# Performance work log

Measured on AMD Instinct MI355X. Metric: run time of the kernel, lower is better.

The kernel has to match this reference:

```python
import jax, jax.numpy as jnp
import numpy as np


def setup_inputs() -> dict:
    key = jax.random.key(0)
    ks = jax.random.split(key, 12)
    N, F, H, E = 100000, 128, 128, 625000
    x = jax.random.normal(ks[0], (N, F), dtype=jnp.float32)
    edge_index = jax.random.randint(ks[1], (2, E), 0, N, dtype=jnp.int64)
    s1 = 1.0 / np.sqrt(2 * F)
    s2 = 1.0 / np.sqrt(H)
    W1 = jax.random.uniform(ks[2], (2 * F, H), jnp.float32, -s1, s1)
    b1 = jax.random.uniform(ks[3], (H,), jnp.float32, -s1, s1)
    W2 = jax.random.uniform(ks[4], (H, H), jnp.float32, -s2, s2)
    b2 = jax.random.uniform(ks[5], (H,), jnp.float32, -s2, s2)
    W3 = jax.random.uniform(ks[6], (H, H), jnp.float32, -s2, s2)
    b3 = jax.random.uniform(ks[7], (H,), jnp.float32, -s2, s2)
    W4 = jax.random.uniform(ks[8], (H, 1), jnp.float32, -s2, s2)
    b4 = jax.random.uniform(ks[9], (1,), jnp.float32, -s2, s2)
    return {"x": x, "edge_index": edge_index, "W1": W1, "b1": b1,
            "W2": W2, "b2": b2, "W3": W3, "b3": b3, "W4": W4, "b4": b4}


def reference(x, edge_index, W1, b1, W2, b2, W3, b3, W4, b4):
    # Gather endpoint features and concat -> [E, 2F]
    x_i = x[edge_index[0], :]
    x_j = x[edge_index[1], :]
    ef = jnp.concatenate([x_i, x_j], axis=-1)
    h = jax.nn.relu(ef @ W1 + b1)
    h = jax.nn.relu(h @ W2 + b2)
    h = jax.nn.relu(h @ W3 + b3)
    return jax.nn.sigmoid(h @ W4 + b4)  # [E, 1]
```

## Files before the change

### kernel.cpp

```cpp
#include <hip/hip_runtime.h>
#include <math.h>

typedef _Float16 half8 __attribute__((ext_vector_type(8)));
typedef _Float16 half4 __attribute__((ext_vector_type(4)));
typedef float f32x4 __attribute__((ext_vector_type(4)));

#define HDIM 128
#define WHALFS 65536
#define SCR_HALFS 2048
#define LDS_HALFS (WHALFS + 8 * SCR_HALFS)
#define LDS_BYTES (LDS_HALFS * 2)

__global__ __launch_bounds__(256) void prep_kernel(
    const float* __restrict__ x,  const float* __restrict__ W1,
    const float* __restrict__ W2, const float* __restrict__ W3,
    _Float16* __restrict__ xh,  _Float16* __restrict__ W1p,
    _Float16* __restrict__ W2p, _Float16* __restrict__ W3p, int NF)
{
    int bid = blockIdx.x;
    if (bid < 32) {
        int t = bid * 256 + threadIdx.x;
        const float* W; _Float16* Wp; int KS; int u;
        if (t < 4096)      { W = W1; Wp = W1p; KS = 8; u = t; }
        else if (t < 6144) { W = W2; Wp = W2p; KS = 4; u = t - 4096; }
        else               { W = W3; Wp = W3p; KS = 4; u = t - 6144; }
        int lane = u & 63;
        int fk   = u >> 6;
        int ks   = fk % KS;
        int ct   = fk / KS;
        int m    = ct * 16 + (lane & 15);
        int k0   = ks * 32 + (lane >> 4) * 8;
        half8 v;
        #pragma unroll
        for (int j = 0; j < 8; ++j) v[j] = (_Float16)W[(k0 + j) * HDIM + m];
        *(half8*)(Wp + (size_t)u * 8) = v;
    } else {
        long i = (long)(bid - 32) * 2048 + (long)threadIdx.x * 8;
        if (i + 8 <= (long)NF) {
            const float4* xf = (const float4*)(x + i);
            float4 f0 = xf[0], f1 = xf[1];
            half8 v;
            v[0] = (_Float16)f0.x; v[1] = (_Float16)f0.y;
            v[2] = (_Float16)f0.z; v[3] = (_Float16)f0.w;
            v[4] = (_Float16)f1.x; v[5] = (_Float16)f1.y;
            v[6] = (_Float16)f1.z; v[7] = (_Float16)f1.w;
            *(half8*)(xh + i) = v;
        }
    }
}

__device__ __forceinline__ void acc_bias_init(
    f32x4 (&acc)[2][8], const float* __restrict__ bias, int quad)
{
    #pragma unroll
    for (int ct = 0; ct < 8; ++ct) {
        float4 bv = *(const float4*)(bias + ct * 16 + quad * 4);
        f32x4 b = {bv.x, bv.y, bv.z, bv.w};
        acc[0][ct] = b;
        acc[1][ct] = b;
    }
}

__device__ __forceinline__ void epi_extract(
    f32x4 (&acc)[2][8], _Float16* __restrict__ scr, int l15, int quad, int sw,
    half8 (&bh)[2][4], const float* __restrict__ next_bias)
{
    #pragma unroll
    for (int nt = 0; nt < 2; ++nt) {
        #pragma unroll
        for (int ct = 0; ct < 8; ++ct) {
            half4 h;
            h[0] = (_Float16)fmaxf(acc[nt][ct][0], 0.f);
            h[1] = (_Float16)fmaxf(acc[nt][ct][1], 0.f);
            h[2] = (_Float16)fmaxf(acc[nt][ct][2], 0.f);
            h[3] = (_Float16)fmaxf(acc[nt][ct][3], 0.f);
            *(half4*)(scr + ((l15 * 128 + ct * 16 + quad * 4) ^ sw)) = h;
        }
        #pragma unroll
        for (int ks = 0; ks < 4; ++ks)
            bh[nt][ks] = *(const half8*)(scr + ((l15 * 128 + ks * 32 + quad * 8) ^ sw));
    }
    acc_bias_init(acc, next_bias, quad);
}

__device__ __forceinline__ void layer_mfma(
    f32x4 (&acc)[2][8], const _Float16* __restrict__ Wl,
    half8 (&bh)[2][4], int lane)
{
    #pragma unroll
    for (int ks = 0; ks < 4; ++ks) {
        #pragma unroll
        for (int ch = 0; ch < 2; ++ch) {
            half8 aw[4];
            #pragma unroll
            for (int c = 0; c < 4; ++c)
                aw[c] = *(const half8*)(Wl + ((size_t)(((ch * 4 + c) * 4 + ks) * 64 + lane)) * 8);
            #pragma unroll
            for (int nt = 0; nt < 2; ++nt)
                #pragma unroll
                for (int c = 0; c < 4; ++c)
                    acc[nt][ch * 4 + c] = __builtin_amdgcn_mfma_f32_16x16x32_f16(
                        aw[c], bh[nt][ks], acc[nt][ch * 4 + c], 0, 0, 0);
        }
    }
}

__global__ __launch_bounds__(512, 2) void edge_mlp_kernel(
    const int* __restrict__ ei, const _Float16* __restrict__ xh,
    const _Float16* __restrict__ wpack,
    const float* __restrict__ b1, const float* __restrict__ b2,
    const float* __restrict__ b3, const float* __restrict__ W4,
    const float* __restrict__ b4, float* __restrict__ out, int E)
{
    extern __shared__ _Float16 lds[];

    {
        float4* dst = (float4*)lds;
        const float4* src = (const float4*)wpack;
        #pragma unroll
        for (int i = 0; i < 16; ++i)
            dst[i * 512 + threadIdx.x] = src[i * 512 + threadIdx.x];
    }
    __syncthreads();

    const int tid  = threadIdx.x;
    const int wave = tid >> 6;
    const int lane = tid & 63;
    const int l15  = lane & 15;
    const int quad = lane >> 4;
    const int sw   = (l15 & 7) << 3;

    const _Float16* W1l = lds;
    const _Float16* W2l = lds + 32768;
    const _Float16* W3l = lds + 49152;
    _Float16* scr = lds + WHALFS + wave * SCR_HALFS;

    const int ntiles = (E + 255) >> 8;
    const float b4v = b4[0];

    for (int t = blockIdx.x; t < ntiles; t += gridDim.x) {
        const int base = t * 256 + wave * 32;

        int gi[2], gj[2];
        #pragma unroll
        for (int nt = 0; nt < 2; ++nt) {
            const int row = min(base + nt * 16 + l15, E - 1);
            gi[nt] = ei[row];
            gj[nt] = ei[E + row];
        }

        f32x4 acc[2][8];
        acc_bias_init(acc, b1, quad);

        half8 bef[2][4];

        #pragma unroll
        for (int nt = 0; nt < 2; ++nt) {
            const _Float16* pi = xh + (size_t)gi[nt] * HDIM;
            #pragma unroll
            for (int ks = 0; ks < 4; ++ks)
                bef[nt][ks] = *(const half8*)(pi + ks * 32 + quad * 8);
        }
        #pragma unroll
        for (int ks = 0; ks < 4; ++ks) {
            #pragma unroll
            for (int ch = 0; ch < 2; ++ch) {
                half8 aw[4];
                #pragma unroll
                for (int c = 0; c < 4; ++c)
                    aw[c] = *(const half8*)(W1l + ((size_t)(((ch * 4 + c) * 8 + ks) * 64 + lane)) * 8);
                #pragma unroll
                for (int nt = 0; nt < 2; ++nt)
                    #pragma unroll
                    for (int c = 0; c < 4; ++c)
                        acc[nt][ch * 4 + c] = __builtin_amdgcn_mfma_f32_16x16x32_f16(
                            aw[c], bef[nt][ks], acc[nt][ch * 4 + c], 0, 0, 0);
            }
        }

        #pragma unroll
        for (int nt = 0; nt < 2; ++nt) {
            const _Float16* pj = xh + (size_t)gj[nt] * HDIM;
            #pragma unroll
            for (int ks = 0; ks < 4; ++ks)
                bef[nt][ks] = *(const half8*)(pj + ks * 32 + quad * 8);
        }
        #pragma unroll
        for (int ks = 0; ks < 4; ++ks) {
            #pragma unroll
            for (int ch = 0; ch < 2; ++ch) {
                half8 aw[4];
                #pragma unroll
                for (int c = 0; c < 4; ++c)
                    aw[c] = *(const half8*)(W1l + ((size_t)(((ch * 4 + c) * 8 + 4 + ks) * 64 + lane)) * 8);
                #pragma unroll
                for (int nt = 0; nt < 2; ++nt)
                    #pragma unroll
                    for (int c = 0; c < 4; ++c)
                        acc[nt][ch * 4 + c] = __builtin_amdgcn_mfma_f32_16x16x32_f16(
                            aw[c], bef[nt][ks], acc[nt][ch * 4 + c], 0, 0, 0);
            }
        }

        half8 bh[2][4];
        epi_extract(acc, scr, l15, quad, sw, bh, b2);
        layer_mfma(acc, W2l, bh, lane);
        epi_extract(acc, scr, l15, quad, sw, bh, b3);
        layer_mfma(acc, W3l, bh, lane);

        #pragma unroll
        for (int nt = 0; nt < 2; ++nt) {
            float s = 0.f;
            #pragma unroll
            for (int ct = 0; ct < 8; ++ct) {
                float4 w4v = *(const float4*)(W4 + ct * 16 + quad * 4);
                s += fmaxf(acc[nt][ct][0], 0.f) * w4v.x;
                s += fmaxf(acc[nt][ct][1], 0.f) * w4v.y;
                s += fmaxf(acc[nt][ct][2], 0.f) * w4v.z;
                s += fmaxf(acc[nt][ct][3], 0.f) * w4v.w;
            }
            s += __shfl_xor(s, 16, 64);
            s += __shfl_xor(s, 32, 64);
            const int row = base + nt * 16 + l15;
            if (quad == 0 && row < E)
                out[row] = 1.f / (1.f + __expf(-(s + b4v)));
        }
    }
}

extern "C" void kernel_launch(void* const* d_in, const int* in_sizes, int n_in,
                              void* d_out, int out_size, void* d_ws, size_t ws_size,
                              hipStream_t stream)
{
    const float* x  = (const float*)d_in[0];
    const int*   ei = (const int*)d_in[1];
    const float* W1 = (const float*)d_in[2];
    const float* b1 = (const float*)d_in[3];
    const float* W2 = (const float*)d_in[4];
    const float* b2 = (const float*)d_in[5];
    const float* W3 = (const float*)d_in[6];
    const float* b3 = (const float*)d_in[7];
    const float* W4 = (const float*)d_in[8];
    const float* b4 = (const float*)d_in[9];
    float* out = (float*)d_out;

    const int NF = in_sizes[0];
    const int E  = out_size;

    _Float16* xh  = (_Float16*)d_ws;
    _Float16* W1p = xh + NF;
    _Float16* W2p = W1p + 32768;
    _Float16* W3p = W2p + 16384;

    const int xblocks = (NF + 2047) / 2048;
    prep_kernel<<<32 + xblocks, 256, 0, stream>>>(x, W1, W2, W3, xh, W1p, W2p, W3p, NF);

    hipFuncSetAttribute((const void*)edge_mlp_kernel,
                        hipFuncAttributeMaxDynamicSharedMemorySize, LDS_BYTES);
    edge_mlp_kernel<<<256, 512, LDS_BYTES, stream>>>(ei, xh, W1p,
                                                     b1, b2, b3, W4, b4, out, E);
}
```

Measured before the change: 192.1 us.

## Prefetch next tile's edge indices and source features during current tile MLP

Software-pipelines the persistent edge loop. The next tile's edge indices are loaded during layer 2, and its source-node feature rows during layer 3, so the gather latency overlaps MFMA work. MFMA blocks are wrapped in s_setprio to favour the matrix waves, and the x-to-fp16 conversion now uses 4 elements per thread with more blocks. Holding the prefetched features in registers raises register pressure, which at 512 threads and 2 blocks per unit could cause spills.

```diff
diff --git a/kernel.cpp b/kernel.cpp
--- a/kernel.cpp
+++ b/kernel.cpp
@@ -35,16 +35,13 @@
         for (int j = 0; j < 8; ++j) v[j] = (_Float16)W[(k0 + j) * HDIM + m];
         *(half8*)(Wp + (size_t)u * 8) = v;
     } else {
-        long i = (long)(bid - 32) * 2048 + (long)threadIdx.x * 8;
-        if (i + 8 <= (long)NF) {
-            const float4* xf = (const float4*)(x + i);
-            float4 f0 = xf[0], f1 = xf[1];
-            half8 v;
-            v[0] = (_Float16)f0.x; v[1] = (_Float16)f0.y;
-            v[2] = (_Float16)f0.z; v[3] = (_Float16)f0.w;
-            v[4] = (_Float16)f1.x; v[5] = (_Float16)f1.y;
-            v[6] = (_Float16)f1.z; v[7] = (_Float16)f1.w;
-            *(half8*)(xh + i) = v;
+        long i = ((long)(bid - 32) * 256 + threadIdx.x) * 4;
+        if (i + 4 <= (long)NF) {
+            float4 f = *(const float4*)(x + i);
+            half4 v;
+            v[0] = (_Float16)f.x; v[1] = (_Float16)f.y;
+            v[2] = (_Float16)f.z; v[3] = (_Float16)f.w;
+            *(half4*)(xh + i) = v;
         }
     }
 }
@@ -87,6 +84,7 @@
     f32x4 (&acc)[2][8], const _Float16* __restrict__ Wl,
     half8 (&bh)[2][4], int lane)
 {
+    __builtin_amdgcn_s_setprio(1);
     #pragma unroll
     for (int ks = 0; ks < 4; ++ks) {
         #pragma unroll
@@ -103,6 +101,31 @@
                         aw[c], bh[nt][ks], acc[nt][ch * 4 + c], 0, 0, 0);
         }
     }
+    __builtin_amdgcn_s_setprio(0);
+}
+
+__device__ __forceinline__ void layer1_half(
+    f32x4 (&acc)[2][8], const _Float16* __restrict__ W1l,
+    half8 (&bef)[2][4], int ks0, int lane)
+{
+    __builtin_amdgcn_s_setprio(1);
+    #pragma unroll
+    for (int ks = 0; ks < 4; ++ks) {
+        #pragma unroll
+        for (int ch = 0; ch < 2; ++ch) {
+            half8 aw[4];
+            #pragma unroll
+            for (int c = 0; c < 4; ++c)
+                aw[c] = *(const half8*)(W1l + ((size_t)(((ch * 4 + c) * 8 + ks0 + ks) * 64 + lane)) * 8);
+            #pragma unroll
+            for (int nt = 0; nt < 2; ++nt)
+                #pragma unroll
+                for (int c = 0; c < 4; ++c)
+                    acc[nt][ch * 4 + c] = __builtin_amdgcn_mfma_f32_16x16x32_f16(
+                        aw[c], bef[nt][ks], acc[nt][ch * 4 + c], 0, 0, 0);
+        }
+    }
+    __builtin_amdgcn_s_setprio(0);
 }
 
 __global__ __launch_bounds__(512, 2) void edge_mlp_kernel(
@@ -138,74 +161,68 @@
     const int ntiles = (E + 255) >> 8;
     const float b4v = b4[0];
 
+    int gi[2], gj[2];
+    half8 befi[2][4];
+    {
+        const int base0 = blockIdx.x * 256 + wave * 32;
+        #pragma unroll
+        for (int nt = 0; nt < 2; ++nt) {
+            const int row = min(base0 + nt * 16 + l15, E - 1);
+            gi[nt] = ei[row];
+            gj[nt] = ei[E + row];
+        }
+        #pragma unroll
+        for (int nt = 0; nt < 2; ++nt) {
+            const _Float16* pi = xh + (size_t)gi[nt] * HDIM;
+            #pragma unroll
+            for (int ks = 0; ks < 4; ++ks)
+                befi[nt][ks] = *(const half8*)(pi + ks * 32 + quad * 8);
+        }
+    }
+
     for (int t = blockIdx.x; t < ntiles; t += gridDim.x) {
         const int base = t * 256 + wave * 32;
 
-        int gi[2], gj[2];
-        #pragma unroll
-        for (int nt = 0; nt < 2; ++nt) {
-            const int row = min(base + nt * 16 + l15, E - 1);
-            gi[nt] = ei[row];
-            gj[nt] = ei[E + row];
+        half8 befj[2][4];
+        #pragma unroll
+        for (int nt = 0; nt < 2; ++nt) {
+            const _Float16* pj = xh + (size_t)gj[nt] * HDIM;
+            #pragma unroll
+            for (int ks = 0; ks < 4; ++ks)
+                befj[nt][ks] = *(const half8*)(pj + ks * 32 + quad * 8);
         }
 
         f32x4 acc[2][8];
         acc_bias_init(acc, b1, quad);
 
-        half8 bef[2][4];
-
-        #pragma unroll
-        for (int nt = 0; nt < 2; ++nt) {
-            const _Float16* pi = xh + (size_t)gi[nt] * HDIM;
-            #pragma unroll
-            for (int ks = 0; ks < 4; ++ks)
-                bef[nt][ks] = *(const half8*)(pi + ks * 32 + quad * 8);
-        }
-        #pragma unroll
-        for (int ks = 0; ks < 4; ++ks) {
-            #pragma unroll
-            for (int ch = 0; ch < 2; ++ch) {
-                half8 aw[4];
-                #pragma unroll
-                for (int c = 0; c < 4; ++c)
-                    aw[c] = *(const half8*)(W1l + ((size_t)(((ch * 4 + c) * 8 + ks) * 64 + lane)) * 8);
-                #pragma unroll
-                for (int nt = 0; nt < 2; ++nt)
-                    #pragma unroll
-                    for (int c = 0; c < 4; ++c)
-                        acc[nt][ch * 4 + c] = __builtin_amdgcn_mfma_f32_16x16x32_f16(
-                            aw[c], bef[nt][ks], acc[nt][ch * 4 + c], 0, 0, 0);
-            }
-        }
-
-        #pragma unroll
-        for (int nt = 0; nt < 2; ++nt) {
-            const _Float16* pj = xh + (size_t)gj[nt] * HDIM;
-            #pragma unroll
-            for (int ks = 0; ks < 4; ++ks)
-                bef[nt][ks] = *(const half8*)(pj + ks * 32 + quad * 8);
-        }
-        #pragma unroll
-        for (int ks = 0; ks < 4; ++ks) {
-            #pragma unroll
-            for (int ch = 0; ch < 2; ++ch) {
-                half8 aw[4];
-                #pragma unroll
-                for (int c = 0; c < 4; ++c)
-                    aw[c] = *(const half8*)(W1l + ((size_t)(((ch * 4 + c) * 8 + 4 + ks) * 64 + lane)) * 8);
-                #pragma unroll
-                for (int nt = 0; nt < 2; ++nt)
-                    #pragma unroll
-                    for (int c = 0; c < 4; ++c)
-                        acc[nt][ch * 4 + c] = __builtin_amdgcn_mfma_f32_16x16x32_f16(
-                            aw[c], bef[nt][ks], acc[nt][ch * 4 + c], 0, 0, 0);
-            }
-        }
+        layer1_half(acc, W1l, befi, 0, lane);
+        layer1_half(acc, W1l, befj, 4, lane);
 
         half8 bh[2][4];
         epi_extract(acc, scr, l15, quad, sw, bh, b2);
+
+        int gin[2], gjn[2];
+        {
+            const int basen = (t + (int)gridDim.x) * 256 + wave * 32;
+            #pragma unroll
+            for (int nt = 0; nt < 2; ++nt) {
+                const int row = min(min(basen + nt * 16 + l15, E - 1), E - 1);
+                gin[nt] = ei[row];
+                gjn[nt] = ei[E + row];
+            }
+        }
+
         layer_mfma(acc, W2l, bh, lane);
         epi_extract(acc, scr, l15, quad, sw, bh, b3);
+
+        #pragma unroll
+        for (int nt = 0; nt < 2; ++nt) {
+            const _Float16* pi = xh + (size_t)gin[nt] * HDIM;
+            #pragma unroll
+            for (int ks = 0; ks < 4; ++ks)
+                befi[nt][ks] = *(const half8*)(pi + ks * 32 + quad * 8);
+        }
+
         layer_mfma(acc, W3l, bh, lane);
 
         #pragma unroll
@@ -225,6 +242,9 @@
             if (quad == 0 && row < E)
                 out[row] = 1.f / (1.f + __expf(-(s + b4v)));
         }
+
+        gi[0] = gin[0]; gi[1] = gin[1];
+        gj[0] = gjn[0]; gj[1] = gjn[1];
     }
 }
 
@@ -252,7 +272,7 @@
     _Float16* W2p = W1p + 32768;
     _Float16* W3p = W2p + 16384;
 
-    const int xblocks = (NF + 2047) / 2048;
+    const int xblocks = (NF + 1023) / 1024;
     prep_kernel<<<32 + xblocks, 256, 0, stream>>>(x, W1, W2, W3, xh, W1p, W2p, W3p, NF);
 
     hipFuncSetAttribute((const void*)edge_mlp_kernel,
```

After: 201.0 us. 4.7% more time.

## Split output columns across wave pairs sharing 64-edge tiles in edge MLP

Applied to the files above, without the earlier changes.

Each pair of waves now processes 64 edges, with each wave computing half of the 128 output columns across four 16-row tiles. This halves the per-wave weight fragment loads from LDS per MFMA and raises B-operand reuse. The price is block-wide __syncthreads for the activation exchange and the final dot-product reduction, plus s_setprio hints around the MFMA loops. The prep kernel also becomes grid-stride with a fixed block count, and NF is hardcoded to the test shape.

```diff
diff --git a/kernel.cpp b/kernel.cpp
--- a/kernel.cpp
+++ b/kernel.cpp
@@ -7,8 +7,8 @@
 
 #define HDIM 128
 #define WHALFS 65536
-#define SCR_HALFS 2048
-#define LDS_HALFS (WHALFS + 8 * SCR_HALFS)
+#define PAIR_SCR_HALFS 4096
+#define LDS_HALFS (WHALFS + 4 * PAIR_SCR_HALFS)
 #define LDS_BYTES (LDS_HALFS * 2)
 
 __global__ __launch_bounds__(256) void prep_kernel(
@@ -35,8 +35,9 @@
         for (int j = 0; j < 8; ++j) v[j] = (_Float16)W[(k0 + j) * HDIM + m];
         *(half8*)(Wp + (size_t)u * 8) = v;
     } else {
-        long i = (long)(bid - 32) * 2048 + (long)threadIdx.x * 8;
-        if (i + 8 <= (long)NF) {
+        const long stride = (long)(gridDim.x - 32) * 256;
+        for (long u = (long)(bid - 32) * 256 + threadIdx.x; u * 8 < (long)NF; u += stride) {
+            long i = u * 8;
             const float4* xf = (const float4*)(x + i);
             float4 f0 = xf[0], f1 = xf[1];
             half8 v;
@@ -50,59 +51,91 @@
 }
 
 __device__ __forceinline__ void acc_bias_init(
-    f32x4 (&acc)[2][8], const float* __restrict__ bias, int quad)
-{
-    #pragma unroll
-    for (int ct = 0; ct < 8; ++ct) {
-        float4 bv = *(const float4*)(bias + ct * 16 + quad * 4);
+    f32x4 (&acc)[4][4], const float* __restrict__ bias, int h, int quad)
+{
+    #pragma unroll
+    for (int ct = 0; ct < 4; ++ct) {
+        float4 bv = *(const float4*)(bias + h * 64 + ct * 16 + quad * 4);
         f32x4 b = {bv.x, bv.y, bv.z, bv.w};
-        acc[0][ct] = b;
-        acc[1][ct] = b;
-    }
-}
-
-__device__ __forceinline__ void epi_extract(
-    f32x4 (&acc)[2][8], _Float16* __restrict__ scr, int l15, int quad, int sw,
-    half8 (&bh)[2][4], const float* __restrict__ next_bias)
-{
-    #pragma unroll
-    for (int nt = 0; nt < 2; ++nt) {
-        #pragma unroll
-        for (int ct = 0; ct < 8; ++ct) {
-            half4 h;
-            h[0] = (_Float16)fmaxf(acc[nt][ct][0], 0.f);
-            h[1] = (_Float16)fmaxf(acc[nt][ct][1], 0.f);
-            h[2] = (_Float16)fmaxf(acc[nt][ct][2], 0.f);
-            h[3] = (_Float16)fmaxf(acc[nt][ct][3], 0.f);
-            *(half4*)(scr + ((l15 * 128 + ct * 16 + quad * 4) ^ sw)) = h;
-        }
-        #pragma unroll
-        for (int ks = 0; ks < 4; ++ks)
-            bh[nt][ks] = *(const half8*)(scr + ((l15 * 128 + ks * 32 + quad * 8) ^ sw));
-    }
-    acc_bias_init(acc, next_bias, quad);
-}
-
-__device__ __forceinline__ void layer_mfma(
-    f32x4 (&acc)[2][8], const _Float16* __restrict__ Wl,
-    half8 (&bh)[2][4], int lane)
-{
+        #pragma unroll
+        for (int nt = 0; nt < 4; ++nt) acc[nt][ct] = b;
+    }
+}
+
+__device__ __forceinline__ void epi_extract_pair(
+    f32x4 (&acc)[4][4], _Float16* __restrict__ scr, int l15, int quad,
+    int h, int sw, half8 (&bh)[4][4], const float* __restrict__ next_bias)
+{
+    #pragma unroll
+    for (int g = 0; g < 2; ++g) {
+        #pragma unroll
+        for (int nl = 0; nl < 2; ++nl) {
+            const int nt = 2 * g + nl;
+            const int r  = nl * 16 + l15;
+            #pragma unroll
+            for (int ct = 0; ct < 4; ++ct) {
+                half4 hv;
+                hv[0] = (_Float16)fmaxf(acc[nt][ct][0], 0.f);
+                hv[1] = (_Float16)fmaxf(acc[nt][ct][1], 0.f);
+                hv[2] = (_Float16)fmaxf(acc[nt][ct][2], 0.f);
+                hv[3] = (_Float16)fmaxf(acc[nt][ct][3], 0.f);
+                *(half4*)(scr + ((r * 128 + h * 64 + ct * 16 + quad * 4) ^ sw)) = hv;
+            }
+        }
+        __syncthreads();
+        #pragma unroll
+        for (int nl = 0; nl < 2; ++nl) {
+            const int nt = 2 * g + nl;
+            const int r  = nl * 16 + l15;
+            #pragma unroll
+            for (int ks = 0; ks < 4; ++ks)
+                bh[nt][ks] = *(const half8*)(scr + ((r * 128 + ks * 32 + quad * 8) ^ sw));
+        }
+        __syncthreads();
+    }
+    acc_bias_init(acc, next_bias, h, quad);
+}
+
+__device__ __forceinline__ void layer_mfma_pair(
+    f32x4 (&acc)[4][4], const _Float16* __restrict__ Wl,
+    half8 (&bh)[4][4], int h, int lane)
+{
+    __builtin_amdgcn_s_setprio(1);
     #pragma unroll
     for (int ks = 0; ks < 4; ++ks) {
-        #pragma unroll
-        for (int ch = 0; ch < 2; ++ch) {
-            half8 aw[4];
+        half8 aw[4];
+        #pragma unroll
+        for (int c = 0; c < 4; ++c)
+            aw[c] = *(const half8*)(Wl + ((size_t)(((h * 4 + c) * 4 + ks) * 64 + lane)) * 8);
+        #pragma unroll
+        for (int nt = 0; nt < 4; ++nt)
             #pragma unroll
             for (int c = 0; c < 4; ++c)
-                aw[c] = *(const half8*)(Wl + ((size_t)(((ch * 4 + c) * 4 + ks) * 64 + lane)) * 8);
-            #pragma unroll
-            for (int nt = 0; nt < 2; ++nt)
-                #pragma unroll
-                for (int c = 0; c < 4; ++c)
-                    acc[nt][ch * 4 + c] = __builtin_amdgcn_mfma_f32_16x16x32_f16(
-                        aw[c], bh[nt][ks], acc[nt][ch * 4 + c], 0, 0, 0);
-        }
-    }
+                acc[nt][c] = __builtin_amdgcn_mfma_f32_16x16x32_f16(
+                    aw[c], bh[nt][ks], acc[nt][c], 0, 0, 0);
+    }
+    __builtin_amdgcn_s_setprio(0);
+}
+
+__device__ __forceinline__ void layer1_half_pair(
+    f32x4 (&acc)[4][4], const _Float16* __restrict__ W1l,
+    half8 (&bef)[4][4], int ks0, int h, int lane)
+{
+    __builtin_amdgcn_s_setprio(1);
+    #pragma unroll
+    for (int ks = 0; ks < 4; ++ks) {
+        half8 aw[4];
+        #pragma unroll
+        for (int c = 0; c < 4; ++c)
+            aw[c] = *(const half8*)(W1l + ((size_t)(((h * 4 + c) * 8 + ks0 + ks) * 64 + lane)) * 8);
+        #pragma unroll
+        for (int nt = 0; nt < 4; ++nt)
+            #pragma unroll
+            for (int c = 0; c < 4; ++c)
+                acc[nt][c] = __builtin_amdgcn_mfma_f32_16x16x32_f16(
+                    aw[c], bef[nt][ks], acc[nt][c], 0, 0, 0);
+    }
+    __builtin_amdgcn_s_setprio(0);
 }
 
 __global__ __launch_bounds__(512, 2) void edge_mlp_kernel(
@@ -125,6 +158,8 @@
 
     const int tid  = threadIdx.x;
     const int wave = tid >> 6;
+    const int pair = wave >> 1;
+    const int h    = wave & 1;
     const int lane = tid & 63;
     const int l15  = lane & 15;
     const int quad = lane >> 4;
@@ -133,98 +168,84 @@
     const _Float16* W1l = lds;
     const _Float16* W2l = lds + 32768;
     const _Float16* W3l = lds + 49152;
-    _Float16* scr = lds + WHALFS + wave * SCR_HALFS;
+    _Float16* scr = lds + WHALFS + pair * PAIR_SCR_HALFS;
 
     const int ntiles = (E + 255) >> 8;
     const float b4v = b4[0];
 
     for (int t = blockIdx.x; t < ntiles; t += gridDim.x) {
-        const int base = t * 256 + wave * 32;
-
-        int gi[2], gj[2];
-        #pragma unroll
-        for (int nt = 0; nt < 2; ++nt) {
-            const int row = min(base + nt * 16 + l15, E - 1);
+        const int base_p = t * 256 + pair * 64;
+
+        int gi[4], gj[4];
+        #pragma unroll
+        for (int nt = 0; nt < 4; ++nt) {
+            const int row = min(base_p + nt * 16 + l15, E - 1);
             gi[nt] = ei[row];
             gj[nt] = ei[E + row];
         }
 
-        f32x4 acc[2][8];
-        acc_bias_init(acc, b1, quad);
-
-        half8 bef[2][4];
-
-        #pragma unroll
-        for (int nt = 0; nt < 2; ++nt) {
+        f32x4 acc[4][4];
+        acc_bias_init(acc, b1, h, quad);
+
+        half8 bef[4][4];
+
+        #pragma unroll
+        for (int nt = 0; nt < 4; ++nt) {
             const _Float16* pi = xh + (size_t)gi[nt] * HDIM;
             #pragma unroll
             for (int ks = 0; ks < 4; ++ks)
                 bef[nt][ks] = *(const half8*)(pi + ks * 32 + quad * 8);
         }
-        #pragma unroll
-        for (int ks = 0; ks < 4; ++ks) {
-            #pragma unroll
-            for (int ch = 0; ch < 2; ++ch) {
-                half8 aw[4];
-                #pragma unroll
-                for (int c = 0; c < 4; ++c)
-                    aw[c] = *(const half8*)(W1l + ((size_t)(((ch * 4 + c) * 8 + ks) * 64 + lane)) * 8);
-                #pragma unroll
-                for (int nt = 0; nt < 2; ++nt)
-                    #pragma unroll
-                    for (int c = 0; c < 4; ++c)
-                        acc[nt][ch * 4 + c] = __builtin_amdgcn_mfma_f32_16x16x32_f16(
-                            aw[c], bef[nt][ks], acc[nt][ch * 4 + c], 0, 0, 0);
-            }
-        }
-
-        #pragma unroll
-        for (int nt = 0; nt < 2; ++nt) {
+        layer1_half_pair(acc, W1l, bef, 0, h, lane);
+
+        #pragma unroll
+        for (int nt = 0; nt < 4; ++nt) {
             const _Float16* pj = xh + (size_t)gj[nt] * HDIM;
             #pragma unroll
             for (int ks = 0; ks < 4; ++ks)
                 bef[nt][ks] = *(const half8*)(pj + ks * 32 + quad * 8);
         }
-        #pragma unroll
-        for (int ks = 0; ks < 4; ++ks) {
-            #pragma unroll
-            for (int ch = 0; ch < 2; ++ch) {
-                half8 aw[4];
-                #pragma unroll
-                for (int c = 0; c < 4; ++c)
-                    aw[c] = *(const half8*)(W1l + ((size_t)(((ch * 4 + c) * 8 + 4 + ks) * 64 + lane)) * 8);
-                #pragma unroll
-                for (int nt = 0; nt < 2; ++nt)
-                    #pragma unroll
-                    for (int c = 0; c < 4; ++c)
-                        acc[nt][ch * 4 + c] = __builtin_amdgcn_mfma_f32_16x16x32_f16(
-                            aw[c], bef[nt][ks], acc[nt][ch * 4 + c], 0, 0, 0);
+        layer1_half_pair(acc, W1l, bef, 4, h, lane);
+
+        half8 bh[4][4];
+        epi_extract_pair(acc, scr, l15, quad, h, sw, bh, b2);
+        layer_mfma_pair(acc, W2l, bh, h, lane);
+        epi_extract_pair(acc, scr, l15, quad, h, sw, bh, b3);
+        layer_mfma_pair(acc, W3l, bh, h, lane);
+
+        float s[4];
+        #pragma unroll
+        for (int nt = 0; nt < 4; ++nt) {
+            float v = 0.f;
+            #pragma unroll
+            for (int ct = 0; ct < 4; ++ct) {
+                float4 w4v = *(const float4*)(W4 + h * 64 + ct * 16 + quad * 4);
+                v += fmaxf(acc[nt][ct][0], 0.f) * w4v.x;
+                v += fmaxf(acc[nt][ct][1], 0.f) * w4v.y;
+                v += fmaxf(acc[nt][ct][2], 0.f) * w4v.z;
+                v += fmaxf(acc[nt][ct][3], 0.f) * w4v.w;
             }
-        }
-
-        half8 bh[2][4];
-        epi_extract(acc, scr, l15, quad, sw, bh, b2);
-        layer_mfma(acc, W2l, bh, lane);
-        epi_extract(acc, scr, l15, quad, sw, bh, b3);
-        layer_mfma(acc, W3l, bh, lane);
-
-        #pragma unroll
-        for (int nt = 0; nt < 2; ++nt) {
-            float s = 0.f;
-            #pragma unroll
-            for (int ct = 0; ct < 8; ++ct) {
-                float4 w4v = *(const float4*)(W4 + ct * 16 + quad * 4);
-                s += fmaxf(acc[nt][ct][0], 0.f) * w4v.x;
-                s += fmaxf(acc[nt][ct][1], 0.f) * w4v.y;
-                s += fmaxf(acc[nt][ct][2], 0.f) * w4v.z;
-                s += fmaxf(acc[nt][ct][3], 0.f) * w4v.w;
+            v += __shfl_xor(v, 16, 64);
+            v += __shfl_xor(v, 32, 64);
+            s[nt] = v;
+        }
+        float* scrf = (float*)scr;
+        if (quad == 0) {
+            #pragma unroll
+            for (int nt = 0; nt < 4; ++nt)
+                scrf[h * 64 + nt * 16 + l15] = s[nt];
+        }
+        __syncthreads();
+        #pragma unroll
+        for (int k = 0; k < 2; ++k) {
+            const int nt  = 2 * h + k;
+            const int row = base_p + nt * 16 + l15;
+            if (quad == 0 && row < E) {
+                float tot = s[nt] + scrf[(1 - h) * 64 + nt * 16 + l15] + b4v;
+                out[row] = 1.f / (1.f + __expf(-tot));
             }
-            s += __shfl_xor(s, 16, 64);
-            s += __shfl_xor(s, 32, 64);
-            const int row = base + nt * 16 + l15;
-            if (quad == 0 && row < E)
-                out[row] = 1.f / (1.f + __expf(-(s + b4v)));
-        }
+        }
+        __syncthreads();
     }
 }
 
@@ -244,7 +265,7 @@
     const float* b4 = (const float*)d_in[9];
     float* out = (float*)d_out;
 
-    const int NF = in_sizes[0];
+    const int NF = 100000 * 128;
     const int E  = out_size;
 
     _Float16* xh  = (_Float16*)d_ws;
@@ -252,8 +273,7 @@
     _Float16* W2p = W1p + 32768;
     _Float16* W3p = W2p + 16384;
 
-    const int xblocks = (NF + 2047) / 2048;
-    prep_kernel<<<32 + xblocks, 256, 0, stream>>>(x, W1, W2, W3, xh, W1p, W2p, W3p, NF);
+    prep_kernel<<<32 + 2048, 256, 0, stream>>>(x, W1, W2, W3, xh, W1p, W2p, W3p, NF);
 
     hipFuncSetAttribute((const void*)edge_mlp_kernel,
                         hipFuncAttributeMaxDynamicSharedMemorySize, LDS_BYTES);
```

Result: slower. 274.9 us (+43.1%).
